# Performance work log

Hardware: AMD Instinct MI355X
Metric: run time of the kernel (lower is better)

## Reference

```python
import jax, jax.numpy as jnp
import numpy as np

B, L, T = 2048, 512, 32


def setup_inputs() -> dict:
    key = jax.random.key(0)
    k1, k2, k3, k4 = jax.random.split(key, 4)
    emit_score = jax.random.normal(k1, (B, L, T), dtype=jnp.float32)
    transition = jax.random.normal(k2, (T, T), dtype=jnp.float32)
    tags = jax.random.randint(k3, (B, L), 0, T, dtype=jnp.int32)
    lengths = jax.random.randint(k4, (B,), 1, L + 1, dtype=jnp.int32)
    return {"emit_score": emit_score, "transition": transition,
            "tags": tags, "lengths": lengths}


def reference(emit_score, transition, tags, lengths):
    # CRF negative log-likelihood (calculate_loss), per-example loss [B].
    b, l, t = emit_score.shape
    mask = jnp.arange(l)[None, :] < lengths[:, None]          # [B,L] bool
    maskf = mask.astype(emit_score.dtype)

    # --- gold path score ---
    gold = jnp.take_along_axis(emit_score, tags[:, :, None], axis=2)[..., 0]  # [B,L]
    trans_gold = transition[tags[:, :-1], tags[:, 1:]]        # [B,L-1]
    gold = gold.at[:, 1:].add(trans_gold)
    total_score = (gold * maskf).sum(axis=1)                  # [B]

    # --- forward algorithm (log partition) via scan over time ---
    emit_tbT = jnp.transpose(emit_score, (1, 0, 2))           # [L,B,T]
    mask_tb = mask.T                                          # [L,B]

    def step(d, x):
        e_t, m_t = x                                          # [B,T], [B]
        # scores[b, prev, next] = d[b,prev] + transition[prev,next] + e_t[b,next]
        scores = d[:, :, None] + transition[None, :, :] + e_t[:, None, :]
        new_d = jax.nn.logsumexp(scores, axis=1)              # [B,T]
        d = jnp.where(m_t[:, None], new_d, d)                 # freeze finished rows
        return d, None

    d0 = emit_tbT[0]                                          # [B,T]
    d, _ = jax.lax.scan(step, d0, (emit_tbT[1:], mask_tb[1:]))
    log_z = jax.nn.logsumexp(d, axis=1)                       # [B]

    return log_z - total_score                                # loss = -llk
```

## Files before the change

kernel.cpp:

```cpp
#include <hip/hip_runtime.h>


constexpr int TT = 32;
constexpr int LL = 512;

#define L2E  1.4426950408889634f
#define LN2f 0.6931471805599453f

template<int X>
__device__ __forceinline__ float swzxf(float v) {
  return __int_as_float(__builtin_amdgcn_ds_swizzle(__float_as_int(v), (X << 10) | 0x1F));
}

__device__ __forceinline__ float rdlanef(float v, int k) {
  return __int_as_float(__builtin_amdgcn_readlane(__float_as_int(v), k));
}

__global__ __launch_bounds__(64) void crf_fwd(
    const float* __restrict__ emit, const float* __restrict__ trans,
    const int* __restrict__ tags, const int* __restrict__ lengths,
    float* __restrict__ out, int B)
{
  __shared__ float s_trans[TT * TT];
  {
    const float4* t4 = (const float4*)trans;
    float4* st4 = (float4*)s_trans;
#pragma unroll
    for (int k = 0; k < 4; ++k)
      st4[threadIdx.x + 64 * k] = t4[threadIdx.x + 64 * k];
  }
  __syncthreads();

  const int j = threadIdx.x & 31;
  const int b = blockIdx.x;
  if (b >= B) return;

  float Ec[TT];
#pragma unroll
  for (int i = 0; i < TT; ++i)
    Ec[i] = __builtin_amdgcn_exp2f(s_trans[i * TT + j] * L2E);

  const int len = lengths[b];
  const float* erow = emit + (size_t)b * (LL * TT);
  const int*  trow  = tags + (size_t)b * LL;

  float e0   = erow[j];
  int   ptag = trow[0];
  float a    = __builtin_amdgcn_exp2f(e0 * L2E);
  float gacc = (j == ptag) ? e0 : 0.f;
  float LS   = 0.f;

  const int nch = (len - 1 + 3) >> 2;

  float eb[4], en[4];
  int   tg[4], tgn[4];
#pragma unroll
  for (int k = 0; k < 4; ++k) {
    int t = 1 + k; int tc = t < LL ? t : LL - 1;
    eb[k] = erow[tc * TT + j];
    tg[k] = trow[tc];
  }
#pragma unroll
  for (int k = 0; k < 4; ++k) {
    int t = 5 + k; int tc = t < LL ? t : LL - 1;
    en[k] = erow[tc * TT + j];
    tgn[k] = trow[tc];
  }

  for (int c = 0; c < nch; ++c) {
    const int tb = 1 + (c << 2);

    float ep[4]; int tgp[4];
#pragma unroll
    for (int k = 0; k < 4; ++k) {
      int t = tb + 8 + k; int tc = t < LL ? t : LL - 1;
      ep[k]  = erow[tc * TT + j];
      tgp[k] = trow[tc];
    }

    float e2v[4];
#pragma unroll
    for (int k = 0; k < 4; ++k) e2v[k] = __builtin_amdgcn_exp2f(eb[k] * L2E);

#pragma unroll
    for (int k = 0; k < 4; ++k) {
      const int t = tb + k;

      float acc0 = 0.f, acc1 = 0.f, acc2 = 0.f, acc3 = 0.f;
#pragma unroll
      for (int q = 0; q < 8; ++q) {
        acc0 = fmaf(rdlanef(a, 4 * q + 0), Ec[4 * q + 0], acc0);
        acc1 = fmaf(rdlanef(a, 4 * q + 1), Ec[4 * q + 1], acc1);
        acc2 = fmaf(rdlanef(a, 4 * q + 2), Ec[4 * q + 2], acc2);
        acc3 = fmaf(rdlanef(a, 4 * q + 3), Ec[4 * q + 3], acc3);
      }
      float anew = ((acc0 + acc1) + (acc2 + acc3)) * e2v[k];
      const bool valid = t < len;
      a = valid ? anew : a;

      int tag  = tg[k];
      float tr = s_trans[(ptag << 5) + j];
      gacc += ((j == tag) && valid) ? (eb[k] + tr) : 0.f;
      ptag = tag;
    }

    float m = fmaxf(__int_as_float(__builtin_amdgcn_readfirstlane(__float_as_int(a))), 1e-30f);
    float r = __builtin_amdgcn_rcpf(m);
    a *= r;
    LS += __builtin_amdgcn_logf(m);

#pragma unroll
    for (int k = 0; k < 4; ++k) {
      eb[k] = en[k]; tg[k] = tgn[k];
      en[k] = ep[k]; tgn[k] = tgp[k];
    }
  }

  float s  = a;
  float gs = gacc;
  s += swzxf<1>(s);   gs += swzxf<1>(gs);
  s += swzxf<2>(s);   gs += swzxf<2>(gs);
  s += swzxf<4>(s);   gs += swzxf<4>(gs);
  s += swzxf<8>(s);   gs += swzxf<8>(gs);
  s += swzxf<16>(s);  gs += swzxf<16>(gs);

  float logz = (__builtin_amdgcn_logf(s) + LS) * LN2f;
  if (threadIdx.x == 0) out[b] = logz - gs;
}

extern "C" void kernel_launch(void* const* d_in, const int* in_sizes, int n_in,
                              void* d_out, int out_size, void* d_ws, size_t ws_size,
                              hipStream_t stream) {
  const float* emit    = (const float*)d_in[0];
  const float* trans   = (const float*)d_in[1];
  const int*   tags    = (const int*)d_in[2];
  const int*   lengths = (const int*)d_in[3];
  float*       out     = (float*)d_out;
  const int B = in_sizes[3];
  hipLaunchKernelGGL(crf_fwd, dim3(B), dim3(64), 0, stream,
                     emit, trans, tags, lengths, out, B);
}
```

Baseline: 337.3 us.

## Restructure CRF forward loop into 8-step chunks with lane-loaded tags and masked tail

The loop now handles 8 timesteps per chunk and ping-pongs between two register buffers instead of rotating three 4-wide buffers. Tags are fetched once per chunk with one lane-per-timestep load and broadcast via readlane, which removes the per-step tag loads and the per-step validity select. The leftover steps run in a separate guarded tail, and launch bounds now ask for 2 waves per SIMD. The change cuts scalar and vector load traffic and per-step branching in the serial recurrence, at the cost of larger unrolled code and higher register pressure.

```diff
diff --git a/kernel.cpp b/kernel.cpp
--- a/kernel.cpp
+++ b/kernel.cpp
@@ -11,12 +11,11 @@
 __device__ __forceinline__ float swzxf(float v) {
   return __int_as_float(__builtin_amdgcn_ds_swizzle(__float_as_int(v), (X << 10) | 0x1F));
 }
-
-__device__ __forceinline__ float rdlanef(float v, int k) {
+__device__ __forceinline__ float rdlf(float v, int k) {
   return __int_as_float(__builtin_amdgcn_readlane(__float_as_int(v), k));
 }
 
-__global__ __launch_bounds__(64) void crf_fwd(
+__global__ __launch_bounds__(64, 2) void crf_fwd(
     const float* __restrict__ emit, const float* __restrict__ trans,
     const int* __restrict__ tags, const int* __restrict__ lengths,
     float* __restrict__ out, int B)
@@ -31,14 +30,17 @@
   }
   __syncthreads();
 
-  const int j = threadIdx.x & 31;
-  const int b = blockIdx.x;
+  const int j    = threadIdx.x & 31;
+  const int lane = threadIdx.x;
+  const int b    = blockIdx.x;
   if (b >= B) return;
 
   float Ec[TT];
 #pragma unroll
   for (int i = 0; i < TT; ++i)
     Ec[i] = __builtin_amdgcn_exp2f(s_trans[i * TT + j] * L2E);
+#pragma unroll
+  for (int i = 0; i < TT; ++i) asm volatile("" : "+v"(Ec[i]));
 
   const int len = lengths[b];
   const float* erow = emit + (size_t)b * (LL * TT);
@@ -50,71 +52,93 @@
   float gacc = (j == ptag) ? e0 : 0.f;
   float LS   = 0.f;
 
-  const int nch = (len - 1 + 3) >> 2;
+  const int nf = (len - 1) >> 3;
+  const int r  = (len - 1) & 7;
 
-  float eb[4], en[4];
-  int   tg[4], tgn[4];
+  float eA[8], eB[8];
+  int tvA, tvB;
 #pragma unroll
-  for (int k = 0; k < 4; ++k) {
-    int t = 1 + k; int tc = t < LL ? t : LL - 1;
-    eb[k] = erow[tc * TT + j];
-    tg[k] = trow[tc];
+  for (int k = 0; k < 8; ++k) { int t = 1 + k; eA[k] = erow[t * TT + j]; }
+  { int t = 1 + lane; t = t < LL ? t : LL - 1; tvA = trow[t]; }
+
+#define STEP(E2_) do {                                                     \
+    float acc0 = 0.f, acc1 = 0.f, acc2 = 0.f, acc3 = 0.f;                  \
+    _Pragma("unroll")                                                      \
+    for (int q = 0; q < 8; ++q) {                                          \
+      acc0 = fmaf(rdlf(a, 4 * q + 0), Ec[4 * q + 0], acc0);                \
+      acc1 = fmaf(rdlf(a, 4 * q + 1), Ec[4 * q + 1], acc1);                \
+      acc2 = fmaf(rdlf(a, 4 * q + 2), Ec[4 * q + 2], acc2);                \
+      acc3 = fmaf(rdlf(a, 4 * q + 3), Ec[4 * q + 3], acc3);                \
+    }                                                                      \
+    a = ((acc0 + acc1) + (acc2 + acc3)) * (E2_);                           \
+  } while (0)
+
+#define RENORM() do {                                                      \
+    float mt = fmaxf(a, 1e-30f);                                           \
+    float m  = __int_as_float(                                             \
+        __builtin_amdgcn_readfirstlane(__float_as_int(mt)));               \
+    a *= __builtin_amdgcn_rcpf(m);                                         \
+    LS += __builtin_amdgcn_logf(m);                                        \
+  } while (0)
+
+#define CHUNK(EC, TVC, EN, TVN, TB) do {                                   \
+    _Pragma("unroll")                                                      \
+    for (int k = 0; k < 8; ++k) {                                          \
+      int t = (TB) + 8 + k; t = t < LL ? t : LL - 1;                       \
+      EN[k] = erow[t * TT + j];                                            \
+    }                                                                      \
+    { int t = (TB) + 8 + lane; t = t < LL ? t : LL - 1; TVN = trow[t]; }   \
+    _Pragma("unroll")                                                      \
+    for (int s = 0; s < 2; ++s) {                                          \
+      const int k0 = 4 * s;                                                \
+      int p0 = (s == 0) ? ptag : __builtin_amdgcn_readlane(TVC, 3);        \
+      int s0 = __builtin_amdgcn_readlane(TVC, k0 + 0);                     \
+      int s1 = __builtin_amdgcn_readlane(TVC, k0 + 1);                     \
+      int s2 = __builtin_amdgcn_readlane(TVC, k0 + 2);                     \
+      int s3 = __builtin_amdgcn_readlane(TVC, k0 + 3);                     \
+      float trv0 = s_trans[(p0 << 5) + j];                                 \
+      float trv1 = s_trans[(s0 << 5) + j];                                 \
+      float trv2 = s_trans[(s1 << 5) + j];                                 \
+      float trv3 = s_trans[(s2 << 5) + j];                                 \
+      float f0 = __builtin_amdgcn_exp2f(EC[k0 + 0] * L2E);                 \
+      float f1 = __builtin_amdgcn_exp2f(EC[k0 + 1] * L2E);                 \
+      float f2 = __builtin_amdgcn_exp2f(EC[k0 + 2] * L2E);                 \
+      float f3 = __builtin_amdgcn_exp2f(EC[k0 + 3] * L2E);                 \
+      STEP(f0); gacc += (j == s0) ? (EC[k0 + 0] + trv0) : 0.f;             \
+      STEP(f1); gacc += (j == s1) ? (EC[k0 + 1] + trv1) : 0.f;             \
+      STEP(f2); gacc += (j == s2) ? (EC[k0 + 2] + trv2) : 0.f;             \
+      STEP(f3); gacc += (j == s3) ? (EC[k0 + 3] + trv3) : 0.f;             \
+      RENORM();                                                            \
+    }                                                                      \
+    ptag = __builtin_amdgcn_readlane(TVC, 7);                              \
+  } while (0)
+
+  int c = 0;
+  for (; c + 2 <= nf; c += 2) {
+    CHUNK(eA, tvA, eB, tvB, 1 + (c << 3));
+    CHUNK(eB, tvB, eA, tvA, 1 + ((c + 1) << 3));
   }
-#pragma unroll
-  for (int k = 0; k < 4; ++k) {
-    int t = 5 + k; int tc = t < LL ? t : LL - 1;
-    en[k] = erow[tc * TT + j];
-    tgn[k] = trow[tc];
+  if (c < nf) {
+    CHUNK(eA, tvA, eB, tvB, 1 + (c << 3));
+    ++c;
   }
 
-  for (int c = 0; c < nch; ++c) {
-    const int tb = 1 + (c << 2);
+#define TAIL(EC, TVC) do {                                                 \
+    _Pragma("unroll")                                                      \
+    for (int k = 0; k < 7; ++k) {                                          \
+      if (k < r) {                                       \
+        int sg = __builtin_amdgcn_readlane(TVC, k);                        \
+        float trv = s_trans[(ptag << 5) + j];                              \
+        float f = __builtin_amdgcn_exp2f(EC[k] * L2E);                     \
+        STEP(f);                                                           \
+        gacc += (j == sg) ? (EC[k] + trv) : 0.f;                           \
+        ptag = sg;                                                         \
+        if (k == 3) RENORM();                                              \
+      }                                                                    \
+    }                                                                      \
+  } while (0)
 
-    float ep[4]; int tgp[4];
-#pragma unroll
-    for (int k = 0; k < 4; ++k) {
-      int t = tb + 8 + k; int tc = t < LL ? t : LL - 1;
-      ep[k]  = erow[tc * TT + j];
-      tgp[k] = trow[tc];
-    }
-
-    float e2v[4];
-#pragma unroll
-    for (int k = 0; k < 4; ++k) e2v[k] = __builtin_amdgcn_exp2f(eb[k] * L2E);
-
-#pragma unroll
-    for (int k = 0; k < 4; ++k) {
-      const int t = tb + k;
-
-      float acc0 = 0.f, acc1 = 0.f, acc2 = 0.f, acc3 = 0.f;
-#pragma unroll
-      for (int q = 0; q < 8; ++q) {
-        acc0 = fmaf(rdlanef(a, 4 * q + 0), Ec[4 * q + 0], acc0);
-        acc1 = fmaf(rdlanef(a, 4 * q + 1), Ec[4 * q + 1], acc1);
-        acc2 = fmaf(rdlanef(a, 4 * q + 2), Ec[4 * q + 2], acc2);
-        acc3 = fmaf(rdlanef(a, 4 * q + 3), Ec[4 * q + 3], acc3);
-      }
-      float anew = ((acc0 + acc1) + (acc2 + acc3)) * e2v[k];
-      const bool valid = t < len;
-      a = valid ? anew : a;
-
-      int tag  = tg[k];
-      float tr = s_trans[(ptag << 5) + j];
-      gacc += ((j == tag) && valid) ? (eb[k] + tr) : 0.f;
-      ptag = tag;
-    }
-
-    float m = fmaxf(__int_as_float(__builtin_amdgcn_readfirstlane(__float_as_int(a))), 1e-30f);
-    float r = __builtin_amdgcn_rcpf(m);
-    a *= r;
-    LS += __builtin_amdgcn_logf(m);
-
-#pragma unroll
-    for (int k = 0; k < 4; ++k) {
-      eb[k] = en[k]; tg[k] = tgn[k];
-      en[k] = ep[k]; tgn[k] = tgp[k];
-    }
-  }
+  if (nf & 1) TAIL(eB, tvB); else TAIL(eA, tvA);
 
   float s  = a;
   float gs = gacc;
```

Measured after the change: 292.6 us. 1.15x faster.

## Split CRF forward recursion into forward and backward halves per sequence

Applied to the files above, without the earlier changes.

Each sequence now runs on two wavefronts: one runs the forward recursion over the first half of the timesteps and the other runs a backward recursion (using the transposed exp-transition matrix) over the second half. The two partial vectors are combined in shared memory by an elementwise product and a sum, which halves the serial dependency chain per sequence. Tags are now loaded as one value per lane and fetched with readlane, and the chunk size grows to 8 steps with renormalisation every 4 steps. The cost is double the per-block registers and threads, a block-wide barrier, and more complex tail handling.

```diff
diff --git a/kernel.cpp b/kernel.cpp
--- a/kernel.cpp
+++ b/kernel.cpp
@@ -11,121 +11,176 @@
 __device__ __forceinline__ float swzxf(float v) {
   return __int_as_float(__builtin_amdgcn_ds_swizzle(__float_as_int(v), (X << 10) | 0x1F));
 }
-
-__device__ __forceinline__ float rdlanef(float v, int k) {
+__device__ __forceinline__ float rdlf(float v, int k) {
   return __int_as_float(__builtin_amdgcn_readlane(__float_as_int(v), k));
 }
 
-__global__ __launch_bounds__(64) void crf_fwd(
+template<int DIR>
+__device__ __forceinline__ void run_dir(
+    const float* __restrict__ erow, const int* __restrict__ trow,
+    const float* s_trans, const float (&Eg)[TT],
+    int j, int ln, int len, int ns,
+    float& a, float& gacc, float& LS)
+{
+  if (ns <= 0) return;
+  const int nf = ns >> 3;
+  const int r  = ns & 7;
+
+  float eA[8], eB[8];
+  int tvA, tvB;
+
+  auto eload = [&](int s) -> float {
+    int t = DIR ? (len - 1 - s) : (1 + s);
+    t = t > 0 ? t : 0;
+    t = t < LL ? t : LL - 1;
+    return erow[t * TT + j];
+  };
+  auto tload = [&](int s0) -> int {
+    int ti = DIR ? (len - 1 - s0 - ln) : (s0 + ln);
+    ti = ti > 0 ? ti : 0;
+    ti = ti < LL ? ti : LL - 1;
+    return trow[ti];
+  };
+  auto dot = [&](float x) -> float {
+    float c0 = 0.f, c1 = 0.f, c2 = 0.f, c3 = 0.f;
+#pragma unroll
+    for (int q = 0; q < 8; ++q) {
+      c0 = fmaf(rdlf(x, 4 * q + 0), Eg[4 * q + 0], c0);
+      c1 = fmaf(rdlf(x, 4 * q + 1), Eg[4 * q + 1], c1);
+      c2 = fmaf(rdlf(x, 4 * q + 2), Eg[4 * q + 2], c2);
+      c3 = fmaf(rdlf(x, 4 * q + 3), Eg[4 * q + 3], c3);
+    }
+    return (c0 + c1) + (c2 + c3);
+  };
+  auto renorm = [&]() {
+    float mt = fmaxf(a, 1e-30f);
+    float m = __int_as_float(__builtin_amdgcn_readfirstlane(__float_as_int(mt)));
+    a *= __builtin_amdgcn_rcpf(m);
+    LS += __builtin_amdgcn_logf(m);
+  };
+
+#define ONESTEP(EC, TVC, K)                                                \
+  {                                                                        \
+    float F = __builtin_amdgcn_exp2f(EC[K] * L2E);                         \
+    int ma = __builtin_amdgcn_readlane(TVC, DIR ? (K) : (K) + 1);          \
+    int pv = __builtin_amdgcn_readlane(TVC, DIR ? (K) + 1 : (K));          \
+    float tr = s_trans[(pv << 5) + j];                                     \
+    if (DIR) a = dot(a * F); else a = dot(a) * F;                          \
+    gacc += (j == ma) ? (EC[K] + tr) : 0.f;                                \
+  }
+
+#define CHUNK(EC, TVC, EN, TVN, S0)                                        \
+  {                                                                        \
+    _Pragma("unroll")                                                      \
+    for (int k = 0; k < 8; ++k) EN[k] = eload((S0) + 8 + k);               \
+    TVN = tload((S0) + 8);                                                 \
+    ONESTEP(EC, TVC, 0) ONESTEP(EC, TVC, 1)                                \
+    ONESTEP(EC, TVC, 2) ONESTEP(EC, TVC, 3)                                \
+    renorm();                                                              \
+    ONESTEP(EC, TVC, 4) ONESTEP(EC, TVC, 5)                                \
+    ONESTEP(EC, TVC, 6) ONESTEP(EC, TVC, 7)                                \
+    renorm();                                                              \
+  }
+
+#pragma unroll
+  for (int k = 0; k < 8; ++k) eA[k] = eload(k);
+  tvA = tload(0);
+
+  int c = 0;
+  for (; c + 2 <= nf; c += 2) {
+    CHUNK(eA, tvA, eB, tvB, (c + 0) << 3);
+    CHUNK(eB, tvB, eA, tvA, (c + 1) << 3);
+  }
+  if (c < nf) {
+    CHUNK(eA, tvA, eB, tvB, c << 3);
+    ++c;
+  }
+
+#define TAIL(EC, TVC)                                                      \
+  {                                                                        \
+    if (0 < r) ONESTEP(EC, TVC, 0)                                         \
+    if (1 < r) ONESTEP(EC, TVC, 1)                                         \
+    if (2 < r) ONESTEP(EC, TVC, 2)                                         \
+    if (3 < r) { ONESTEP(EC, TVC, 3) renorm(); }                           \
+    if (4 < r) ONESTEP(EC, TVC, 4)                                         \
+    if (5 < r) ONESTEP(EC, TVC, 5)                                         \
+    if (6 < r) ONESTEP(EC, TVC, 6)                                         \
+  }
+
+  if (nf & 1) TAIL(eB, tvB) else TAIL(eA, tvA)
+
+#undef ONESTEP
+#undef CHUNK
+#undef TAIL
+}
+
+__global__ __launch_bounds__(128, 4) void crf_fwd(
     const float* __restrict__ emit, const float* __restrict__ trans,
     const int* __restrict__ tags, const int* __restrict__ lengths,
     float* __restrict__ out, int B)
 {
   __shared__ float s_trans[TT * TT];
+  __shared__ float s_vec[2][TT];
+  __shared__ float s_scl[2][2];
   {
     const float4* t4 = (const float4*)trans;
     float4* st4 = (float4*)s_trans;
-#pragma unroll
-    for (int k = 0; k < 4; ++k)
-      st4[threadIdx.x + 64 * k] = t4[threadIdx.x + 64 * k];
+    st4[threadIdx.x]       = t4[threadIdx.x];
+    st4[threadIdx.x + 128] = t4[threadIdx.x + 128];
   }
   __syncthreads();
 
-  const int j = threadIdx.x & 31;
-  const int b = blockIdx.x;
-  if (b >= B) return;
+  const int j  = threadIdx.x & 31;
+  const int ln = threadIdx.x & 63;
+  const int wv = threadIdx.x >> 6;
+  const int b  = blockIdx.x;
 
-  float Ec[TT];
+  float Eg[TT];
 #pragma unroll
-  for (int i = 0; i < TT; ++i)
-    Ec[i] = __builtin_amdgcn_exp2f(s_trans[i * TT + j] * L2E);
+  for (int i = 0; i < TT; ++i) {
+    int idx = wv ? (j * TT + i) : (i * TT + j);
+    Eg[i] = __builtin_amdgcn_exp2f(s_trans[idx] * L2E);
+  }
+#pragma unroll
+  for (int i = 0; i < TT; ++i) asm volatile("" : "+v"(Eg[i]));
 
   const int len = lengths[b];
+  const int m   = (len - 1) >> 1;
+  const int ns  = wv ? (len - 1 - m) : m;
   const float* erow = emit + (size_t)b * (LL * TT);
-  const int*  trow  = tags + (size_t)b * LL;
+  const int*   trow = tags + (size_t)b * LL;
 
-  float e0   = erow[j];
-  int   ptag = trow[0];
-  float a    = __builtin_amdgcn_exp2f(e0 * L2E);
-  float gacc = (j == ptag) ? e0 : 0.f;
-  float LS   = 0.f;
-
-  const int nch = (len - 1 + 3) >> 2;
-
-  float eb[4], en[4];
-  int   tg[4], tgn[4];
-#pragma unroll
-  for (int k = 0; k < 4; ++k) {
-    int t = 1 + k; int tc = t < LL ? t : LL - 1;
-    eb[k] = erow[tc * TT + j];
-    tg[k] = trow[tc];
-  }
-#pragma unroll
-  for (int k = 0; k < 4; ++k) {
-    int t = 5 + k; int tc = t < LL ? t : LL - 1;
-    en[k] = erow[tc * TT + j];
-    tgn[k] = trow[tc];
+  float a, gacc, LS = 0.f;
+  if (wv == 0) {
+    float e0 = erow[j];
+    int   t0 = trow[0];
+    a    = __builtin_amdgcn_exp2f(e0 * L2E);
+    gacc = (j == t0) ? e0 : 0.f;
+  } else {
+    a    = 1.f;
+    gacc = 0.f;
   }
 
-  for (int c = 0; c < nch; ++c) {
-    const int tb = 1 + (c << 2);
+  if (wv == 0)
+    run_dir<0>(erow, trow, s_trans, Eg, j, ln, len, ns, a, gacc, LS);
+  else
+    run_dir<1>(erow, trow, s_trans, Eg, j, ln, len, ns, a, gacc, LS);
 
-    float ep[4]; int tgp[4];
-#pragma unroll
-    for (int k = 0; k < 4; ++k) {
-      int t = tb + 8 + k; int tc = t < LL ? t : LL - 1;
-      ep[k]  = erow[tc * TT + j];
-      tgp[k] = trow[tc];
-    }
+  float gs = gacc;
+  gs += swzxf<1>(gs);  gs += swzxf<2>(gs);  gs += swzxf<4>(gs);
+  gs += swzxf<8>(gs);  gs += swzxf<16>(gs);
 
-    float e2v[4];
-#pragma unroll
-    for (int k = 0; k < 4; ++k) e2v[k] = __builtin_amdgcn_exp2f(eb[k] * L2E);
+  s_vec[wv][j] = a;
+  if (ln == 0) { s_scl[wv][0] = gs; s_scl[wv][1] = LS; }
+  __syncthreads();
 
-#pragma unroll
-    for (int k = 0; k < 4; ++k) {
-      const int t = tb + k;
-
-      float acc0 = 0.f, acc1 = 0.f, acc2 = 0.f, acc3 = 0.f;
-#pragma unroll
-      for (int q = 0; q < 8; ++q) {
-        acc0 = fmaf(rdlanef(a, 4 * q + 0), Ec[4 * q + 0], acc0);
-        acc1 = fmaf(rdlanef(a, 4 * q + 1), Ec[4 * q + 1], acc1);
-        acc2 = fmaf(rdlanef(a, 4 * q + 2), Ec[4 * q + 2], acc2);
-        acc3 = fmaf(rdlanef(a, 4 * q + 3), Ec[4 * q + 3], acc3);
-      }
-      float anew = ((acc0 + acc1) + (acc2 + acc3)) * e2v[k];
-      const bool valid = t < len;
-      a = valid ? anew : a;
-
-      int tag  = tg[k];
-      float tr = s_trans[(ptag << 5) + j];
-      gacc += ((j == tag) && valid) ? (eb[k] + tr) : 0.f;
-      ptag = tag;
-    }
-
-    float m = fmaxf(__int_as_float(__builtin_amdgcn_readfirstlane(__float_as_int(a))), 1e-30f);
-    float r = __builtin_amdgcn_rcpf(m);
-    a *= r;
-    LS += __builtin_amdgcn_logf(m);
-
-#pragma unroll
-    for (int k = 0; k < 4; ++k) {
-      eb[k] = en[k]; tg[k] = tgn[k];
-      en[k] = ep[k]; tgn[k] = tgp[k];
-    }
+  if (wv == 0) {
+    float p = s_vec[0][j] * s_vec[1][j];
+    p += swzxf<1>(p);  p += swzxf<2>(p);  p += swzxf<4>(p);
+    p += swzxf<8>(p);  p += swzxf<16>(p);
+    float logz = (__builtin_amdgcn_logf(p) + s_scl[0][1] + s_scl[1][1]) * LN2f;
+    if (threadIdx.x == 0) out[b] = logz - (s_scl[0][0] + s_scl[1][0]);
   }
-
-  float s  = a;
-  float gs = gacc;
-  s += swzxf<1>(s);   gs += swzxf<1>(gs);
-  s += swzxf<2>(s);   gs += swzxf<2>(gs);
-  s += swzxf<4>(s);   gs += swzxf<4>(gs);
-  s += swzxf<8>(s);   gs += swzxf<8>(gs);
-  s += swzxf<16>(s);  gs += swzxf<16>(gs);
-
-  float logz = (__builtin_amdgcn_logf(s) + LS) * LN2f;
-  if (threadIdx.x == 0) out[b] = logz - gs;
 }
 
 extern "C" void kernel_launch(void* const* d_in, const int* in_sizes, int n_in,
@@ -137,6 +192,6 @@
   const int*   lengths = (const int*)d_in[3];
   float*       out     = (float*)d_out;
   const int B = in_sizes[3];
-  hipLaunchKernelGGL(crf_fwd, dim3(B), dim3(64), 0, stream,
+  hipLaunchKernelGGL(crf_fwd, dim3(B), dim3(128), 0, stream,
                      emit, trans, tags, lengths, out, B);
 }
```

New measurement: 278.6 us. 1.21x faster.
